# Performance work log

Measured on AMD Instinct MI355X. Metric: run time of the kernel, lower is better.

Reference implementation:

```python
import jax, jax.numpy as jnp
import numpy as np


def conv2d(x, w, b, pad):
    y = jax.lax.conv_general_dilated(x, w, (1, 1), [(pad, pad), (pad, pad)],
                                     dimension_numbers=('NCHW', 'OIHW', 'NCHW'))
    return y + b[None, :, None, None]


def setup_inputs() -> dict:
    key = jax.random.key(0)
    ks = jax.random.split(key, 24)
    bs, C, OC, K = 2, 64, 3, 3
    hi = wi = 96
    ho = wo = 192

    def _w(k, o, i, kh, kw):
        return jax.random.normal(k, (o, i, kh, kw), jnp.float32) / np.float32(np.sqrt(i * kh * kw))

    inp = {
        'x': jax.random.normal(ks[0], (bs, C, hi, wi), jnp.float32),
        'poseMap': jax.random.normal(ks[1], (1, 3, ho, wo), jnp.float32),
        'interMapY': jax.random.randint(ks[2], (ho, wo), 0, hi, jnp.int32),
        'interMapX': jax.random.randint(ks[3], (ho, wo), 0, wi, jnp.int32),
        # sigmaconv: 3x3 convs 64->64->64->2
        'sig_w1': _w(ks[4], 64, 64, 3, 3), 'sig_b1': jnp.zeros((64,), jnp.float32),
        'sig_w2': _w(ks[5], 64, 64, 3, 3), 'sig_b2': jnp.zeros((64,), jnp.float32),
        'sig_w3': _w(ks[6], 2, 64, 3, 3), 'sig_b3': jnp.zeros((2,), jnp.float32),
        # dwconv: 1x1 convs 3->64->256->C*K*K
        'dw_w1': _w(ks[7], 64, 3, 1, 1), 'dw_b1': jnp.zeros((64,), jnp.float32),
        'dw_w2': _w(ks[8], 256, 64, 1, 1), 'dw_b2': jnp.zeros((256,), jnp.float32),
        'dw_w3': _w(ks[9], C * K * K, 256, 1, 1), 'dw_b3': jnp.zeros((C * K * K,), jnp.float32),
        # pwconv: 1x1 convs 3->64->256->C*OC
        'pw_w1': _w(ks[10], 64, 3, 1, 1), 'pw_b1': jnp.zeros((64,), jnp.float32),
        'pw_w2': _w(ks[11], 256, 64, 1, 1), 'pw_b2': jnp.zeros((256,), jnp.float32),
        'pw_w3': _w(ks[12], C * OC, 256, 1, 1), 'pw_b3': jnp.zeros((C * OC,), jnp.float32),
    }
    return inp


def reference(x, poseMap, interMapY, interMapX,
              sig_w1, sig_b1, sig_w2, sig_b2, sig_w3, sig_b3,
              dw_w1, dw_b1, dw_w2, dw_b2, dw_w3, dw_b3,
              pw_w1, pw_b1, pw_w2, pw_b2, pw_w3, pw_b3):
    C, K, OC = 64, 3, 3
    bs, _, hi, wi = x.shape
    ho, wo = poseMap.shape[2], poseMap.shape[3]
    pad = K // 2

    p = jax.lax.stop_gradient(poseMap)  # original detaches poseMap
    # kernel-predict branches (1x1 conv MLPs over position map)
    dw = conv2d(jax.nn.relu(conv2d(jax.nn.relu(conv2d(p, dw_w1, dw_b1, 0)), dw_w2, dw_b2, 0)), dw_w3, dw_b3, 0)
    dw = dw.reshape(1, C, K * K, ho, wo)
    pw = conv2d(jax.nn.relu(conv2d(jax.nn.relu(conv2d(p, pw_w1, pw_b1, 0)), pw_w2, pw_b2, 0)), pw_w3, pw_b3, 0)
    pw = pw.reshape(C, OC, ho, wo)

    # unfold(x, K, padding=K//2): [bs, C, K*K, hi, wi], kernel taps row-major
    xp = jnp.pad(x, ((0, 0), (0, 0), (pad, pad), (pad, pad)))
    h = jnp.stack([xp[:, :, dy:dy + hi, dx:dx + wi]
                   for dy in range(K) for dx in range(K)], axis=2)
    # irregular spatial gather to HR grid: [bs, C, K*K, ho, wo]
    h = h[:, :, :, interMapY, interMapX]

    mean = jnp.sum(h * jax.nn.softmax(dw, axis=2), axis=2)  # [bs, C, ho, wo]
    sigma = conv2d(jax.nn.relu(conv2d(jax.nn.relu(conv2d(mean, sig_w1, sig_b1, 1)), sig_w2, sig_b2, 1)), sig_w3, sig_b3, 1)
    sigmad = sigma[:, 0:1, None, :, :]
    sigmar = sigma[:, 1:2, None, :, :]
    bw = sigmad * dw + sigmar * jnp.abs(h - mean[:, :, None, :, :])
    xa = jnp.sum(h * jax.nn.softmax(bw, axis=2), axis=2)  # [bs, C, ho, wo]
    out = jnp.einsum('bchw,cohw->bohw', xa, pw)  # [bs, OC, ho, wo]
    return out
```

## Files before the change

kernel.cpp:

```cpp
#include <hip/hip_runtime.h>

#define NPIX 36864

typedef __attribute__((ext_vector_type(8))) short short8;
typedef __attribute__((ext_vector_type(4))) short short4v;
typedef __attribute__((ext_vector_type(4))) float float4v;

__device__ inline unsigned short f2b(float x) {
    unsigned int u = __float_as_uint(x);
    unsigned int r = (u + 0x7FFFu + ((u >> 16) & 1u)) >> 16;
    return (unsigned short)r;
}
__device__ inline float b2f(unsigned short h) {
    return __uint_as_float(((unsigned int)h) << 16);
}

#define WB_TOTAL 312320
#define XCAST_N  1179648
__global__ __launch_bounds__(256) void prep_all(
    const float* __restrict__ dw2, const float* __restrict__ dw3,
    const float* __restrict__ pw2, const float* __restrict__ pw3,
    const float* __restrict__ sw1, const float* __restrict__ sw2,
    const float* __restrict__ sw3, unsigned short* __restrict__ wb,
    const float* __restrict__ x, unsigned short* __restrict__ xb)
{
    int i = blockIdx.x * 256 + threadIdx.x;
    if (i >= WB_TOTAL) {
        int j = i - WB_TOTAL;
        if (j < XCAST_N) xb[j] = f2b(x[j]);
        return;
    }
    unsigned short v;
    if (i < 16384)        v = f2b(dw2[i]);
    else if (i < 32768)   v = f2b(pw2[i - 16384]);
    else if (i < 180224)  v = f2b(dw3[i - 32768]);
    else if (i < 229376)  v = f2b(pw3[i - 180224]);
    else if (i < 266240) { int j = i - 229376; int t = j / 4096, r = j % 4096, oc = r / 64, ic = r % 64;
                           v = f2b(sw1[(oc * 64 + ic) * 9 + t]); }
    else if (i < 303104) { int j = i - 266240; int t = j / 4096, r = j % 4096, oc = r / 64, ic = r % 64;
                           v = f2b(sw2[(oc * 64 + ic) * 9 + t]); }
    else                 { int j = i - 303104; int t = j / 1024, r = j % 1024, oc = r / 64, ic = r % 64;
                           v = (oc < 2) ? f2b(sw3[(oc * 64 + ic) * 9 + t]) : (unsigned short)0; }
    wb[i] = v;
}

__global__ __launch_bounds__(256) void mlp_fused(
    const float* __restrict__ pose,
    const float* __restrict__ w1A, const float* __restrict__ b1A,
    const float* __restrict__ w1B, const float* __restrict__ b1B,
    const unsigned short* __restrict__ w2A, const unsigned short* __restrict__ w2B,
    const float* __restrict__ b2A, const float* __restrict__ b2B,
    const unsigned short* __restrict__ w33,
    const float* __restrict__ b3A, const float* __restrict__ b3B,
    unsigned short* __restrict__ outA, unsigned short* __restrict__ outB)
{
    __shared__ unsigned short sh[64 * 264 + 64 * 72];
    unsigned short* h2s = sh;
    unsigned short* h1s = sh + 64 * 264;
    unsigned short* Ts  = h1s;
    const int tid = threadIdx.x;
    const int u = blockIdx.y;
    const int chain = (u == 3) ? 1 : 0;
    const int px0 = blockIdx.x * 64;
    const int w = tid >> 6, l = tid & 63;
    const int ln = l & 15, lkg = l >> 4, lk = lkg * 8;
    const float* w1 = chain ? w1B : w1A;
    const float* b1 = chain ? b1B : b1A;
    const unsigned short* w2 = chain ? w2B : w2A;
    const float* b2 = chain ? b2B : b2A;
    {
        int px = px0 + l;
        float p0 = pose[px], p1 = pose[NPIX + px], p2 = pose[2 * NPIX + px];
        #pragma unroll
        for (int j = 0; j < 16; ++j) {
            int oc = w * 16 + j;
            float v = b1[oc] + w1[oc * 3] * p0 + w1[oc * 3 + 1] * p1 + w1[oc * 3 + 2] * p2;
            h1s[l * 72 + oc] = f2b(fmaxf(v, 0.f));
        }
    }
    __syncthreads();
    {
        float4v acc[4][4] = {};
        #pragma unroll
        for (int mt = 0; mt < 4; ++mt) {
            int ocr = w * 64 + mt * 16 + ln;
            short8 a0 = *(const short8*)&w2[(size_t)ocr * 64 + lk];
            short8 a1 = *(const short8*)&w2[(size_t)ocr * 64 + 32 + lk];
            #pragma unroll
            for (int nt = 0; nt < 4; ++nt) {
                short8 b0 = *(const short8*)&h1s[(nt * 16 + ln) * 72 + lk];
                short8 b1v = *(const short8*)&h1s[(nt * 16 + ln) * 72 + 32 + lk];
                acc[mt][nt] = __builtin_amdgcn_mfma_f32_16x16x32_bf16(a0, b0, acc[mt][nt], 0, 0, 0);
                acc[mt][nt] = __builtin_amdgcn_mfma_f32_16x16x32_bf16(a1, b1v, acc[mt][nt], 0, 0, 0);
            }
        }
        #pragma unroll
        for (int mt = 0; mt < 4; ++mt) {
            int ocb = w * 64 + mt * 16 + lkg * 4;
            float bv0 = b2[ocb + 0], bv1 = b2[ocb + 1], bv2 = b2[ocb + 2], bv3 = b2[ocb + 3];
            #pragma unroll
            for (int nt = 0; nt < 4; ++nt) {
                int pxl = nt * 16 + ln;
                h2s[pxl * 264 + ocb + 0] = f2b(fmaxf(acc[mt][nt][0] + bv0, 0.f));
                h2s[pxl * 264 + ocb + 1] = f2b(fmaxf(acc[mt][nt][1] + bv1, 0.f));
                h2s[pxl * 264 + ocb + 2] = f2b(fmaxf(acc[mt][nt][2] + bv2, 0.f));
                h2s[pxl * 264 + ocb + 3] = f2b(fmaxf(acc[mt][nt][3] + bv3, 0.f));
            }
        }
    }
    __syncthreads();
    const int rowbase = chain ? 576 : u * 192;
    const int obase   = chain ? 0 : u * 192;
    const float* b3 = chain ? b3B : b3A;
    unsigned short* outp = chain ? outB : outA;
    float4v acc[3][4] = {};
    const int r0 = rowbase + w * 48 + ln;
    #pragma unroll
    for (int kc = 0; kc < 8; ++kc) {
        short8 a0 = *(const short8*)&w33[(size_t)(r0 +  0) * 256 + kc * 32 + lk];
        short8 a1 = *(const short8*)&w33[(size_t)(r0 + 16) * 256 + kc * 32 + lk];
        short8 a2 = *(const short8*)&w33[(size_t)(r0 + 32) * 256 + kc * 32 + lk];
        #pragma unroll
        for (int nt = 0; nt < 4; ++nt) {
            short8 b = *(const short8*)&h2s[(nt * 16 + ln) * 264 + kc * 32 + lk];
            acc[0][nt] = __builtin_amdgcn_mfma_f32_16x16x32_bf16(a0, b, acc[0][nt], 0, 0, 0);
            acc[1][nt] = __builtin_amdgcn_mfma_f32_16x16x32_bf16(a1, b, acc[1][nt], 0, 0, 0);
            acc[2][nt] = __builtin_amdgcn_mfma_f32_16x16x32_bf16(a2, b, acc[2][nt], 0, 0, 0);
        }
    }
    #pragma unroll
    for (int mt = 0; mt < 3; ++mt) {
        __syncthreads();
        {
            int tr = w * 16 + lkg * 4;
            #pragma unroll
            for (int r = 0; r < 4; ++r) {
                float bv = b3[obase + w * 48 + mt * 16 + lkg * 4 + r];
                #pragma unroll
                for (int nt = 0; nt < 4; ++nt)
                    Ts[(tr + r) * 72 + nt * 16 + ln] = f2b(acc[mt][nt][r] + bv);
            }
        }
        __syncthreads();
        for (int i = tid; i < 512; i += 256) {
            int row = i >> 3, pc = (i & 7) * 8;
            int gr = obase + (row >> 4) * 48 + mt * 16 + (row & 15);
            *(short8*)&outp[(size_t)gr * NPIX + px0 + pc] = *(const short8*)&Ts[row * 72 + pc];
        }
    }
}

template<int MT>
__global__ __launch_bounds__(256) void conv3x3_mfma(
    const unsigned short* __restrict__ act, const unsigned short* __restrict__ wgt,
    const float* __restrict__ bias, unsigned short* __restrict__ out,
    int relu)
{
    constexpr int SP = 72;
    constexpr int OCP = MT * 16;
    __shared__ unsigned short Bs[3 * 66 * SP];
    const int tid = threadIdx.x;
    int bx = blockIdx.x;
    const int xt = bx % 3; bx /= 3;
    const int y = bx % 192; const int b = bx / 192;
    const int x0 = xt * 64;
    const size_t actb = (size_t)b * NPIX * 64;
    const int w = tid >> 6, l = tid & 63;
    const int ln = l & 15, lkg = l >> 4, lk = lkg * 8;
    const int mt = (MT == 4) ? w : 0;
    short8 Wr[9][2];
    #pragma unroll
    for (int t = 0; t < 9; ++t)
        #pragma unroll
        for (int hh = 0; hh < 2; ++hh)
            Wr[t][hh] = *(const short8*)&wgt[((size_t)t * OCP + mt * 16 + ln) * 64 + hh * 32 + lk];
    for (int s = tid; s < 198; s += 256) {
        int r = s / 66, i = s % 66;
        int yy = y + r - 1, xx = x0 + i - 1;
        unsigned short* dst = &Bs[(r * 66 + i) * SP];
        if (yy >= 0 && yy < 192 && xx >= 0 && xx < 192) {
            const unsigned short* src = &act[actb + (size_t)(yy * 192 + xx) * 64];
            #pragma unroll
            for (int j = 0; j < 8; ++j) *(short8*)(dst + j * 8) = *(const short8*)(src + j * 8);
        } else {
            short8 z = {};
            #pragma unroll
            for (int j = 0; j < 8; ++j) *(short8*)(dst + j * 8) = z;
        }
    }
    __syncthreads();
    const int NT = (MT == 4) ? 4 : 1;
    const int ntb = (MT == 4) ? 0 : w;
    float4v acc[4] = {{0,0,0,0},{0,0,0,0},{0,0,0,0},{0,0,0,0}};
    #pragma unroll
    for (int t = 0; t < 9; ++t) {
        const int r = t / 3, dx = t % 3;
        #pragma unroll
        for (int hh = 0; hh < 2; ++hh) {
            #pragma unroll
            for (int n = 0; n < 4; ++n) {
                if (n >= NT) break;
                int slot = r * 66 + (ntb + n) * 16 + ln + dx;
                short8 bf = *(const short8*)&Bs[slot * SP + hh * 32 + lk];
                acc[n] = __builtin_amdgcn_mfma_f32_16x16x32_bf16(Wr[t][hh], bf, acc[n], 0, 0, 0);
            }
        }
    }
    #pragma unroll
    for (int n = 0; n < 4; ++n) {
        if (n >= NT) break;
        int px = y * 192 + x0 + (ntb + n) * 16 + ln;
        if (MT == 4) {
            int oc = mt * 16 + lkg * 4;
            float v0 = acc[n][0] + bias[oc + 0];
            float v1 = acc[n][1] + bias[oc + 1];
            float v2 = acc[n][2] + bias[oc + 2];
            float v3 = acc[n][3] + bias[oc + 3];
            if (relu) { v0 = fmaxf(v0, 0.f); v1 = fmaxf(v1, 0.f); v2 = fmaxf(v2, 0.f); v3 = fmaxf(v3, 0.f); }
            uint2 pk;
            pk.x = (unsigned int)f2b(v0) | (((unsigned int)f2b(v1)) << 16);
            pk.y = (unsigned int)f2b(v2) | (((unsigned int)f2b(v3)) << 16);
            *(uint2*)&out[((size_t)b * NPIX + px) * 64 + oc] = pk;
        } else if (lkg == 0) {
            float v0 = acc[n][0] + bias[0];
            float v1 = acc[n][1] + bias[1];
            out[((size_t)b * 2 + 0) * NPIX + px] = f2b(v0);
            out[((size_t)b * 2 + 1) * NPIX + px] = f2b(v1);
        }
    }
}

#define PLSZ 10192
__device__ inline void stage_planes(const unsigned short* __restrict__ xb, int c,
                                    unsigned short* __restrict__ pl, int tid)
{
    short8 z = {};
    short8* pf = (short8*)pl;
    for (int i = tid; i < (2 * PLSZ) / 8; i += 256) pf[i] = z;
    __syncthreads();
    #pragma unroll
    for (int b = 0; b < 2; ++b) {
        const unsigned short* xp = xb + (size_t)(b * 64 + c) * 9216;
        unsigned short* pb = pl + b * PLSZ;
        for (int i = tid; i < 96 * 12; i += 256) {
            int row = i / 12, ch = i % 12;
            const short4v* src = (const short4v*)&xp[row * 96 + ch * 8];
            unsigned short* d = &pb[(row + 1) * 104 + 4 + ch * 8];
            *(short4v*)d = src[0];
            *(short4v*)(d + 4) = src[1];
        }
    }
    __syncthreads();
}

__global__ __launch_bounds__(256) void mean_k(
    const unsigned short* __restrict__ xb, const int* __restrict__ imy, const int* __restrict__ imx,
    const unsigned short* __restrict__ dw, unsigned short* __restrict__ mean_cm)
{
    __shared__ unsigned short pl[2 * PLSZ];
    const int c = blockIdx.y;
    const int px0 = blockIdx.x * 1024;
    const int tid = threadIdx.x;
    stage_planes(xb, c, pl, tid);
    #pragma unroll
    for (int q = 0; q < 4; ++q) {
        int px = px0 + q * 256 + tid;
        int base = imy[px] * 104 + imx[px] + 3;
        float wk[9];
        {
            float d[9];
            #pragma unroll
            for (int k = 0; k < 9; ++k) d[k] = b2f(dw[(size_t)(c * 9 + k) * NPIX + px]);
            float m = d[0];
            #pragma unroll
            for (int k = 1; k < 9; ++k) m = fmaxf(m, d[k]);
            float s = 0.f;
            #pragma unroll
            for (int k = 0; k < 9; ++k) { wk[k] = __expf(d[k] - m); s += wk[k]; }
            float inv = 1.f / s;
            #pragma unroll
            for (int k = 0; k < 9; ++k) wk[k] *= inv;
        }
        #pragma unroll
        for (int b = 0; b < 2; ++b) {
            const unsigned short* pb = pl + b * PLSZ;
            float a = 0.f;
            #pragma unroll
            for (int k = 0; k < 9; ++k)
                a += wk[k] * b2f(pb[base + (k / 3) * 104 + (k % 3)]);
            mean_cm[(size_t)(b * 64 + c) * NPIX + px] = f2b(a);
        }
    }
}

__global__ __launch_bounds__(256) void tr_k(
    const unsigned short* __restrict__ in, unsigned short* __restrict__ out)
{
    __shared__ unsigned short T[64 * 68];
    int px0 = blockIdx.x * 64;
    int b = blockIdx.y;
    int tid = threadIdx.x;
    for (int i = tid; i < 4096; i += 256) {
        int c = i >> 6, p = i & 63;
        T[p * 68 + c] = in[(size_t)(b * 64 + c) * NPIX + px0 + p];
    }
    __syncthreads();
    for (int i = tid; i < 4096; i += 256) {
        int p = i >> 6, c = i & 63;
        out[((size_t)b * NPIX + px0 + p) * 64 + c] = T[p * 68 + c];
    }
}

__global__ __launch_bounds__(256) void xa_k(
    const unsigned short* __restrict__ xb, const int* __restrict__ imy, const int* __restrict__ imx,
    const unsigned short* __restrict__ dw, const unsigned short* __restrict__ mean_cm,
    const unsigned short* __restrict__ sigma, unsigned short* __restrict__ xab)
{
    __shared__ unsigned short pl[2 * PLSZ];
    const int c = blockIdx.y;
    const int px0 = blockIdx.x * 1024;
    const int tid = threadIdx.x;
    stage_planes(xb, c, pl, tid);
    #pragma unroll
    for (int q = 0; q < 4; ++q) {
        int px = px0 + q * 256 + tid;
        int base = imy[px] * 104 + imx[px] + 3;
        float d[9];
        #pragma unroll
        for (int k = 0; k < 9; ++k) d[k] = b2f(dw[(size_t)(c * 9 + k) * NPIX + px]);
        #pragma unroll
        for (int b = 0; b < 2; ++b) {
            const unsigned short* pb = pl + b * PLSZ;
            float mn = b2f(mean_cm[(size_t)(b * 64 + c) * NPIX + px]);
            float sd = b2f(sigma[((size_t)b * 2 + 0) * NPIX + px]);
            float sr = b2f(sigma[((size_t)b * 2 + 1) * NPIX + px]);
            float h[9], bw[9];
            #pragma unroll
            for (int k = 0; k < 9; ++k) {
                h[k] = b2f(pb[base + (k / 3) * 104 + (k % 3)]);
                bw[k] = sd * d[k] + sr * fabsf(h[k] - mn);
            }
            float m = bw[0];
            #pragma unroll
            for (int k = 1; k < 9; ++k) m = fmaxf(m, bw[k]);
            float s = 0.f, a = 0.f;
            #pragma unroll
            for (int k = 0; k < 9; ++k) { float e = __expf(bw[k] - m); s += e; a += e * h[k]; }
            xab[(size_t)(b * 64 + c) * NPIX + px] = f2b(a / s);
        }
    }
}

__global__ __launch_bounds__(256) void einsum_part(
    const unsigned short* __restrict__ xab, const unsigned short* __restrict__ pw,
    float* __restrict__ part)
{
    int px = blockIdx.x * 256 + threadIdx.x;
    int b = blockIdx.y;
    int c0 = blockIdx.z * 16;
    float a0 = 0.f, a1 = 0.f, a2 = 0.f;
    #pragma unroll
    for (int c = 0; c < 16; ++c) {
        float v = b2f(xab[(size_t)(b * 64 + c0 + c) * NPIX + px]);
        a0 += v * b2f(pw[(size_t)((c0 + c) * 3 + 0) * NPIX + px]);
        a1 += v * b2f(pw[(size_t)((c0 + c) * 3 + 1) * NPIX + px]);
        a2 += v * b2f(pw[(size_t)((c0 + c) * 3 + 2) * NPIX + px]);
    }
    size_t base = ((size_t)blockIdx.z * 6 + b * 3) * NPIX + px;
    part[base + 0 * NPIX] = a0;
    part[base + 1 * NPIX] = a1;
    part[base + 2 * NPIX] = a2;
}

__global__ __launch_bounds__(256) void einsum_red(
    const float* __restrict__ part, float* __restrict__ out)
{
    int i = blockIdx.x * 256 + threadIdx.x;
    float s = part[i] + part[(size_t)6 * NPIX + i] + part[(size_t)12 * NPIX + i] + part[(size_t)18 * NPIX + i];
    out[i] = s;
}

extern "C" void kernel_launch(void* const* d_in, const int* in_sizes, int n_in,
                              void* d_out, int out_size, void* d_ws, size_t ws_size,
                              hipStream_t stream)
{
    (void)in_sizes; (void)n_in; (void)out_size; (void)ws_size;
    const float* x      = (const float*)d_in[0];
    const float* pose   = (const float*)d_in[1];
    const int*   imy    = (const int*)d_in[2];
    const int*   imx    = (const int*)d_in[3];
    const float* sig_w1 = (const float*)d_in[4];
    const float* sig_b1 = (const float*)d_in[5];
    const float* sig_w2 = (const float*)d_in[6];
    const float* sig_b2 = (const float*)d_in[7];
    const float* sig_w3 = (const float*)d_in[8];
    const float* sig_b3 = (const float*)d_in[9];
    const float* dw_w1  = (const float*)d_in[10];
    const float* dw_b1  = (const float*)d_in[11];
    const float* dw_w2  = (const float*)d_in[12];
    const float* dw_b2  = (const float*)d_in[13];
    const float* dw_w3  = (const float*)d_in[14];
    const float* dw_b3  = (const float*)d_in[15];
    const float* pw_w1  = (const float*)d_in[16];
    const float* pw_b1  = (const float*)d_in[17];
    const float* pw_w2  = (const float*)d_in[18];
    const float* pw_b2  = (const float*)d_in[19];
    const float* pw_w3  = (const float*)d_in[20];
    const float* pw_b3  = (const float*)d_in[21];
    float* out = (float*)d_out;

    unsigned short* ws = (unsigned short*)d_ws;
    size_t off = 0;
    unsigned short* wb      = ws + off; off += WB_TOTAL;
    unsigned short* xb16    = ws + off; off += (size_t)XCAST_N;
    unsigned short* dwbuf   = ws + off; off += (size_t)576 * NPIX;
    unsigned short* pwbuf   = ws + off; off += (size_t)192 * NPIX;
    unsigned short* mean_cm = ws + off; off += (size_t)2 * 64 * NPIX;
    unsigned short* mean_pm = ws + off; off += (size_t)2 * NPIX * 64;
    unsigned short* s1      = ws + off; off += (size_t)2 * NPIX * 64;
    unsigned short* s2      = ws + off; off += (size_t)2 * NPIX * 64;
    unsigned short* sigma   = ws + off; off += (size_t)2 * 2 * NPIX;
    unsigned short* xab     = ws + off; off += (size_t)2 * 64 * NPIX;
    off = (off + 1) & ~(size_t)1;
    float* part = (float*)(ws + off);

    unsigned short* w_dw2 = wb + 0;
    unsigned short* w_pw2 = wb + 16384;
    unsigned short* w_33  = wb + 32768;
    unsigned short* w_s1t = wb + 229376;
    unsigned short* w_s2t = wb + 266240;
    unsigned short* w_s3t = wb + 303104;

    dim3 blk(256);
    prep_all<<<dim3((WB_TOTAL + XCAST_N + 255) / 256), blk, 0, stream>>>(
        dw_w2, dw_w3, pw_w2, pw_w3, sig_w1, sig_w2, sig_w3, wb, x, xb16);
    mlp_fused<<<dim3(576, 4), blk, 0, stream>>>(
        pose, dw_w1, dw_b1, pw_w1, pw_b1, w_dw2, w_pw2, dw_b2, pw_b2,
        w_33, dw_b3, pw_b3, dwbuf, pwbuf);
    mean_k<<<dim3(36, 64), blk, 0, stream>>>(xb16, imy, imx, dwbuf, mean_cm);
    tr_k<<<dim3(576, 2), blk, 0, stream>>>(mean_cm, mean_pm);
    conv3x3_mfma<4><<<dim3(1152), blk, 0, stream>>>(mean_pm, w_s1t, sig_b1, s1, 1);
    conv3x3_mfma<4><<<dim3(1152), blk, 0, stream>>>(s1,      w_s2t, sig_b2, s2, 1);
    conv3x3_mfma<1><<<dim3(1152), blk, 0, stream>>>(s2,      w_s3t, sig_b3, sigma, 0);
    xa_k<<<dim3(36, 64), blk, 0, stream>>>(xb16, imy, imx, dwbuf, mean_cm, sigma, xab);
    einsum_part<<<dim3(144, 2, 4), blk, 0, stream>>>(xab, pwbuf, part);
    einsum_red<<<dim3(864), blk, 0, stream>>>(part, out);
}
```

Before: 259.5 us.

## Compute two output rows per conv3x3 block and re-layout MLP shared buffers

The 3x3 conv kernels now compute two output rows per block, staging a 4-row halo instead of 3 and halving the grid. This reuses the per-block weight register loads and the overlapping halo rows across both outputs. The MLP kernel's shared-memory activations move to a chunked [k-chunk][pixel][8] layout with vectorized stores and hoisted B-fragment loads, aimed at fewer LDS bank conflicts and fewer LDS instructions. In exchange the conv grid has fewer blocks (576), which may lower occupancy, and the MLP needs an extra barrier.

```diff
diff --git a/kernel.cpp b/kernel.cpp
--- a/kernel.cpp
+++ b/kernel.cpp
@@ -54,9 +54,9 @@
     const float* __restrict__ b3A, const float* __restrict__ b3B,
     unsigned short* __restrict__ outA, unsigned short* __restrict__ outB)
 {
-    __shared__ unsigned short sh[64 * 264 + 64 * 72];
+    __shared__ unsigned short sh[32 * 512 + 4608];
     unsigned short* h2s = sh;
-    unsigned short* h1s = sh + 64 * 264;
+    unsigned short* h1s = sh + 32 * 512;
     unsigned short* Ts  = h1s;
     const int tid = threadIdx.x;
     const int u = blockIdx.y;
@@ -71,15 +71,25 @@
     {
         int px = px0 + l;
         float p0 = pose[px], p1 = pose[NPIX + px], p2 = pose[2 * NPIX + px];
+        short8 s0, s1;
         #pragma unroll
         for (int j = 0; j < 16; ++j) {
             int oc = w * 16 + j;
             float v = b1[oc] + w1[oc * 3] * p0 + w1[oc * 3 + 1] * p1 + w1[oc * 3 + 2] * p2;
-            h1s[l * 72 + oc] = f2b(fmaxf(v, 0.f));
-        }
+            unsigned short uv = f2b(fmaxf(v, 0.f));
+            if (j < 8) s0[j] = (short)uv; else s1[j - 8] = (short)uv;
+        }
+        *(short8*)&h1s[(w * 2 + 0) * 512 + l * 8] = s0;
+        *(short8*)&h1s[(w * 2 + 1) * 512 + l * 8] = s1;
     }
     __syncthreads();
     {
+        short8 b0v[4], b1v[4];
+        #pragma unroll
+        for (int nt = 0; nt < 4; ++nt) {
+            b0v[nt] = *(const short8*)&h1s[(lkg    ) * 512 + (nt * 16 + ln) * 8];
+            b1v[nt] = *(const short8*)&h1s[(4 + lkg) * 512 + (nt * 16 + ln) * 8];
+        }
         float4v acc[4][4] = {};
         #pragma unroll
         for (int mt = 0; mt < 4; ++mt) {
@@ -88,23 +98,25 @@
             short8 a1 = *(const short8*)&w2[(size_t)ocr * 64 + 32 + lk];
             #pragma unroll
             for (int nt = 0; nt < 4; ++nt) {
-                short8 b0 = *(const short8*)&h1s[(nt * 16 + ln) * 72 + lk];
-                short8 b1v = *(const short8*)&h1s[(nt * 16 + ln) * 72 + 32 + lk];
-                acc[mt][nt] = __builtin_amdgcn_mfma_f32_16x16x32_bf16(a0, b0, acc[mt][nt], 0, 0, 0);
-                acc[mt][nt] = __builtin_amdgcn_mfma_f32_16x16x32_bf16(a1, b1v, acc[mt][nt], 0, 0, 0);
-            }
-        }
+                acc[mt][nt] = __builtin_amdgcn_mfma_f32_16x16x32_bf16(a0, b0v[nt], acc[mt][nt], 0, 0, 0);
+                acc[mt][nt] = __builtin_amdgcn_mfma_f32_16x16x32_bf16(a1, b1v[nt], acc[mt][nt], 0, 0, 0);
+            }
+        }
+        __syncthreads();
         #pragma unroll
         for (int mt = 0; mt < 4; ++mt) {
             int ocb = w * 64 + mt * 16 + lkg * 4;
+            int chk = ocb >> 3, pos = (lkg & 1) * 4;
             float bv0 = b2[ocb + 0], bv1 = b2[ocb + 1], bv2 = b2[ocb + 2], bv3 = b2[ocb + 3];
             #pragma unroll
             for (int nt = 0; nt < 4; ++nt) {
                 int pxl = nt * 16 + ln;
-                h2s[pxl * 264 + ocb + 0] = f2b(fmaxf(acc[mt][nt][0] + bv0, 0.f));
-                h2s[pxl * 264 + ocb + 1] = f2b(fmaxf(acc[mt][nt][1] + bv1, 0.f));
-                h2s[pxl * 264 + ocb + 2] = f2b(fmaxf(acc[mt][nt][2] + bv2, 0.f));
-                h2s[pxl * 264 + ocb + 3] = f2b(fmaxf(acc[mt][nt][3] + bv3, 0.f));
+                short4v pk;
+                pk[0] = (short)f2b(fmaxf(acc[mt][nt][0] + bv0, 0.f));
+                pk[1] = (short)f2b(fmaxf(acc[mt][nt][1] + bv1, 0.f));
+                pk[2] = (short)f2b(fmaxf(acc[mt][nt][2] + bv2, 0.f));
+                pk[3] = (short)f2b(fmaxf(acc[mt][nt][3] + bv3, 0.f));
+                *(short4v*)&h2s[chk * 512 + pxl * 8 + pos] = pk;
             }
         }
     }
@@ -122,7 +134,7 @@
         short8 a2 = *(const short8*)&w33[(size_t)(r0 + 32) * 256 + kc * 32 + lk];
         #pragma unroll
         for (int nt = 0; nt < 4; ++nt) {
-            short8 b = *(const short8*)&h2s[(nt * 16 + ln) * 264 + kc * 32 + lk];
+            short8 b = *(const short8*)&h2s[(kc * 4 + lkg) * 512 + (nt * 16 + ln) * 8];
             acc[0][nt] = __builtin_amdgcn_mfma_f32_16x16x32_bf16(a0, b, acc[0][nt], 0, 0, 0);
             acc[1][nt] = __builtin_amdgcn_mfma_f32_16x16x32_bf16(a1, b, acc[1][nt], 0, 0, 0);
             acc[2][nt] = __builtin_amdgcn_mfma_f32_16x16x32_bf16(a2, b, acc[2][nt], 0, 0, 0);
@@ -158,11 +170,12 @@
 {
     constexpr int SP = 72;
     constexpr int OCP = MT * 16;
-    __shared__ unsigned short Bs[3 * 66 * SP];
+    __shared__ unsigned short Bs[4 * 66 * SP];
     const int tid = threadIdx.x;
     int bx = blockIdx.x;
     const int xt = bx % 3; bx /= 3;
-    const int y = bx % 192; const int b = bx / 192;
+    const int yg = bx % 96; const int b = bx / 96;
+    const int y0 = yg * 2;
     const int x0 = xt * 64;
     const size_t actb = (size_t)b * NPIX * 64;
     const int w = tid >> 6, l = tid & 63;
@@ -174,9 +187,9 @@
         #pragma unroll
         for (int hh = 0; hh < 2; ++hh)
             Wr[t][hh] = *(const short8*)&wgt[((size_t)t * OCP + mt * 16 + ln) * 64 + hh * 32 + lk];
-    for (int s = tid; s < 198; s += 256) {
+    for (int s = tid; s < 264; s += 256) {
         int r = s / 66, i = s % 66;
-        int yy = y + r - 1, xx = x0 + i - 1;
+        int yy = y0 + r - 1, xx = x0 + i - 1;
         unsigned short* dst = &Bs[(r * 66 + i) * SP];
         if (yy >= 0 && yy < 192 && xx >= 0 && xx < 192) {
             const unsigned short* src = &act[actb + (size_t)(yy * 192 + xx) * 64];
@@ -191,41 +204,47 @@
     __syncthreads();
     const int NT = (MT == 4) ? 4 : 1;
     const int ntb = (MT == 4) ? 0 : w;
-    float4v acc[4] = {{0,0,0,0},{0,0,0,0},{0,0,0,0},{0,0,0,0}};
+    float4v acc[2][4] = {};
     #pragma unroll
     for (int t = 0; t < 9; ++t) {
         const int r = t / 3, dx = t % 3;
         #pragma unroll
         for (int hh = 0; hh < 2; ++hh) {
             #pragma unroll
-            for (int n = 0; n < 4; ++n) {
-                if (n >= NT) break;
-                int slot = r * 66 + (ntb + n) * 16 + ln + dx;
-                short8 bf = *(const short8*)&Bs[slot * SP + hh * 32 + lk];
-                acc[n] = __builtin_amdgcn_mfma_f32_16x16x32_bf16(Wr[t][hh], bf, acc[n], 0, 0, 0);
-            }
-        }
-    }
-    #pragma unroll
-    for (int n = 0; n < 4; ++n) {
-        if (n >= NT) break;
-        int px = y * 192 + x0 + (ntb + n) * 16 + ln;
-        if (MT == 4) {
-            int oc = mt * 16 + lkg * 4;
-            float v0 = acc[n][0] + bias[oc + 0];
-            float v1 = acc[n][1] + bias[oc + 1];
-            float v2 = acc[n][2] + bias[oc + 2];
-            float v3 = acc[n][3] + bias[oc + 3];
-            if (relu) { v0 = fmaxf(v0, 0.f); v1 = fmaxf(v1, 0.f); v2 = fmaxf(v2, 0.f); v3 = fmaxf(v3, 0.f); }
-            uint2 pk;
-            pk.x = (unsigned int)f2b(v0) | (((unsigned int)f2b(v1)) << 16);
-            pk.y = (unsigned int)f2b(v2) | (((unsigned int)f2b(v3)) << 16);
-            *(uint2*)&out[((size_t)b * NPIX + px) * 64 + oc] = pk;
-        } else if (lkg == 0) {
-            float v0 = acc[n][0] + bias[0];
-            float v1 = acc[n][1] + bias[1];
-            out[((size_t)b * 2 + 0) * NPIX + px] = f2b(v0);
-            out[((size_t)b * 2 + 1) * NPIX + px] = f2b(v1);
+            for (int o = 0; o < 2; ++o) {
+                #pragma unroll
+                for (int n = 0; n < 4; ++n) {
+                    if (n >= NT) break;
+                    int slot = (o + r) * 66 + (ntb + n) * 16 + ln + dx;
+                    short8 bf = *(const short8*)&Bs[slot * SP + hh * 32 + lk];
+                    acc[o][n] = __builtin_amdgcn_mfma_f32_16x16x32_bf16(Wr[t][hh], bf, acc[o][n], 0, 0, 0);
+                }
+            }
+        }
+    }
+    #pragma unroll
+    for (int o = 0; o < 2; ++o) {
+        #pragma unroll
+        for (int n = 0; n < 4; ++n) {
+            if (n >= NT) break;
+            int px = (y0 + o) * 192 + x0 + (ntb + n) * 16 + ln;
+            if (MT == 4) {
+                int oc = mt * 16 + lkg * 4;
+                float v0 = acc[o][n][0] + bias[oc + 0];
+                float v1 = acc[o][n][1] + bias[oc + 1];
+                float v2 = acc[o][n][2] + bias[oc + 2];
+                float v3 = acc[o][n][3] + bias[oc + 3];
+                if (relu) { v0 = fmaxf(v0, 0.f); v1 = fmaxf(v1, 0.f); v2 = fmaxf(v2, 0.f); v3 = fmaxf(v3, 0.f); }
+                uint2 pk;
+                pk.x = (unsigned int)f2b(v0) | (((unsigned int)f2b(v1)) << 16);
+                pk.y = (unsigned int)f2b(v2) | (((unsigned int)f2b(v3)) << 16);
+                *(uint2*)&out[((size_t)b * NPIX + px) * 64 + oc] = pk;
+            } else if (lkg == 0) {
+                float v0 = acc[o][n][0] + bias[0];
+                float v1 = acc[o][n][1] + bias[1];
+                out[((size_t)b * 2 + 0) * NPIX + px] = f2b(v0);
+                out[((size_t)b * 2 + 1) * NPIX + px] = f2b(v1);
+            }
         }
     }
 }
@@ -439,9 +458,9 @@
         w_33, dw_b3, pw_b3, dwbuf, pwbuf);
     mean_k<<<dim3(36, 64), blk, 0, stream>>>(xb16, imy, imx, dwbuf, mean_cm);
     tr_k<<<dim3(576, 2), blk, 0, stream>>>(mean_cm, mean_pm);
-    conv3x3_mfma<4><<<dim3(1152), blk, 0, stream>>>(mean_pm, w_s1t, sig_b1, s1, 1);
-    conv3x3_mfma<4><<<dim3(1152), blk, 0, stream>>>(s1,      w_s2t, sig_b2, s2, 1);
-    conv3x3_mfma<1><<<dim3(1152), blk, 0, stream>>>(s2,      w_s3t, sig_b3, sigma, 0);
+    conv3x3_mfma<4><<<dim3(576), blk, 0, stream>>>(mean_pm, w_s1t, sig_b1, s1, 1);
+    conv3x3_mfma<4><<<dim3(576), blk, 0, stream>>>(s1,      w_s2t, sig_b2, s2, 1);
+    conv3x3_mfma<1><<<dim3(576), blk, 0, stream>>>(s2,      w_s3t, sig_b3, sigma, 0);
     xa_k<<<dim3(36, 64), blk, 0, stream>>>(xb16, imy, imx, dwbuf, mean_cm, sigma, xab);
     einsum_part<<<dim3(144, 2, 4), blk, 0, stream>>>(xab, pwbuf, part);
     einsum_red<<<dim3(864), blk, 0, stream>>>(part, out);
```

Result: faster. 251.7 us (-3.0%).
